# Kernel tuning notes

Measured on AMD Instinct MI355X. Metric: run time of the kernel, lower is better.

The kernel has to match this reference:

```python
import jax, jax.numpy as jnp
import numpy as np

D_IN = 2048
D_LATENT = 16384
BATCH = 4096
K = 64


def setup_inputs() -> dict:
    key = jax.random.key(0)
    k1, k2, k3 = jax.random.split(key, 3)
    s_enc = 1.0 / np.sqrt(D_IN)
    s_dec = 1.0 / np.sqrt(D_LATENT)
    return {
        "x": jax.random.normal(k1, (BATCH, D_IN), dtype=jnp.float32),
        "W_enc": jax.random.normal(k2, (D_LATENT, D_IN), dtype=jnp.float32) * s_enc,
        "b_enc": jnp.zeros((D_LATENT,), dtype=jnp.float32),
        "W_dec": jax.random.normal(k3, (D_IN, D_LATENT), dtype=jnp.float32) * s_dec,
        "b_dec": jnp.zeros((D_IN,), dtype=jnp.float32),
        "k": K,
    }


def reference(x, W_enc, b_enc, W_dec, b_dec, k):
    # encode: dense GEMM + ReLU  -> h: [B, d_latent]
    h = jax.nn.relu(jnp.einsum("bd,ld->bl", x, W_enc) + b_enc)
    # top-k masking over latent dim (dim=1)
    _, idx = jax.lax.top_k(h, k)  # idx: [B, k]
    B = h.shape[0]
    mask = jnp.zeros(h.shape, dtype=bool).at[jnp.arange(B)[:, None], idx].set(True)
    h_topk = jnp.where(mask, h, jnp.zeros((), dtype=h.dtype))
    # decode: GEMM through sparse latents
    x_hat = jnp.einsum("bl,dl->bd", h_topk, W_dec) + b_dec
    return x_hat, h, h_topk
```

## Files before the change

### kernel.cpp

```cpp
#include <hip/hip_runtime.h>
#include <cstdint>

#define DIN   2048
#define DLAT  16384
#define NB    4096
#define KSEL  64
#define MAXC  128
#define CAP   2048
#define SEG   64
#define TAU   1.5f

typedef unsigned short u16;
typedef unsigned int   u32;
typedef __attribute__((ext_vector_type(8))) short short8;
typedef __attribute__((ext_vector_type(4))) float f32x4;
typedef __attribute__((ext_vector_type(4))) u32  u32x4;

#define GLOAD_LDS16(g, l)                                              \
    __builtin_amdgcn_global_load_lds(                                  \
        (const __attribute__((address_space(1))) void*)(g),            \
        (__attribute__((address_space(3))) void*)(l), 16, 0, 0)

__device__ __forceinline__ u32 f32_to_bf16(u32 u)
{
    u += 0x7FFFu + ((u >> 16) & 1u);
    return u >> 16;
}

__device__ __forceinline__ float bf16_to_f32(u16 w)
{
    return __uint_as_float((u32)w << 16);
}

__global__ __launch_bounds__(256)
void cvt_f32_bf16_kernel(const float* __restrict__ in, u16* __restrict__ out, int n8)
{
    const int i = blockIdx.x * 256 + threadIdx.x;
    if (i >= n8) return;
    const float4* p = reinterpret_cast<const float4*>(in) + (size_t)i * 2;
    const float4 a = p[0], b = p[1];
    const float v[8] = {a.x, a.y, a.z, a.w, b.x, b.y, b.z, b.w};
    u32 r[8];
#pragma unroll
    for (int j = 0; j < 8; ++j) r[j] = f32_to_bf16(__float_as_uint(v[j]));
    uint4 o;
    o.x = r[0] | (r[1] << 16);
    o.y = r[2] | (r[3] << 16);
    o.z = r[4] | (r[5] << 16);
    o.w = r[6] | (r[7] << 16);
    reinterpret_cast<uint4*>(out)[i] = o;
}

template <bool APPEND>
__global__ __launch_bounds__(512, 2)
void sae_encode_8ph(const u16* __restrict__ XB, const u16* __restrict__ WB,
                    const float* __restrict__ benc, float* __restrict__ H,
                    u32* __restrict__ cnt2, uint2* __restrict__ candbase)
{
    __shared__ __align__(16) u16 lds[65536];

    const int tid = threadIdx.x;
    const int wv  = tid >> 6;
    const int ln  = tid & 63;
    const int wm  = wv >> 2;
    const int wn  = wv & 3;
    const int fr  = ln & 15;
    const int fq  = ln >> 4;

    const int b   = blockIdx.x;
    const int wg  = (b & 7) * 128 + (b >> 3);
    const int m_blk = wg & 15;
    const int n_blk = wg >> 4;
    const size_t bm = (size_t)m_blk * 256;
    const size_t bn = (size_t)n_blk * 256;

    const int sslot = (ln & 3) ^ ((ln >> 3) & 3);
    const int srow  = wv * 16 + (ln >> 2);
    const u16* aSrc = XB + (bm + srow) * (size_t)DIN + sslot * 8;
    const u16* bSrc = WB + (bn + srow) * (size_t)DIN + sslot * 8;
    const size_t rowStep = (size_t)128 * DIN;

    auto STG = [&](int mat, int tile, int kkh) {
        const u16* s0 = (mat ? bSrc : aSrc) + tile * 64 + kkh * 32;
        const int dst = (tile & 1) * 32768 + mat * 16384 + kkh * 8192 + wv * 512;
        GLOAD_LDS16(s0,           &lds[dst]);
        GLOAD_LDS16(s0 + rowStep, &lds[dst + 4096]);
    };

    f32x4 acc[8][4];
#pragma unroll
    for (int i = 0; i < 8; ++i)
#pragma unroll
        for (int j = 0; j < 4; ++j) acc[i][j] = (f32x4)0.0f;

    const int swb = (fq ^ ((fr >> 1) & 3)) * 8;
    const int arow0 = wm * 128 + fr;
    const int brow0 = wn * 64 + fr;

    STG(0, 0, 0); STG(1, 0, 0);
    STG(0, 0, 1); STG(1, 0, 1);
    STG(0, 1, 0); STG(1, 1, 0);

    short8 aR[8], bX[2], bY[2];

    for (int g = 0; g < 32; ++g) {
        const int buf = (g & 1) * 32768;

        if (g < 31) asm volatile("s_waitcnt vmcnt(8)" ::: "memory");
        else        asm volatile("s_waitcnt vmcnt(4)" ::: "memory");
        __builtin_amdgcn_s_barrier();
#pragma unroll
        for (int mi = 0; mi < 8; ++mi)
            aR[mi] = *reinterpret_cast<const short8*>(
                &lds[buf + (arow0 + mi * 16) * 32 + swb]);
        bX[0] = *reinterpret_cast<const short8*>(&lds[buf + 16384 + (brow0 +  0) * 32 + swb]);
        bX[1] = *reinterpret_cast<const short8*>(&lds[buf + 16384 + (brow0 + 16) * 32 + swb]);
        if (g < 31) { STG(0, g + 1, 1); STG(1, g + 1, 1); }
        asm volatile("s_waitcnt lgkmcnt(0)" ::: "memory");
        __builtin_amdgcn_sched_barrier(0);
        __builtin_amdgcn_s_setprio(1);
#pragma unroll
        for (int mi = 0; mi < 8; ++mi) {
            acc[mi][0] = __builtin_amdgcn_mfma_f32_16x16x32_bf16(aR[mi], bX[0], acc[mi][0], 0, 0, 0);
            acc[mi][1] = __builtin_amdgcn_mfma_f32_16x16x32_bf16(aR[mi], bX[1], acc[mi][1], 0, 0, 0);
        }
        __builtin_amdgcn_s_setprio(0);

        __builtin_amdgcn_s_barrier();
        bY[0] = *reinterpret_cast<const short8*>(&lds[buf + 16384 + (brow0 + 32) * 32 + swb]);
        bY[1] = *reinterpret_cast<const short8*>(&lds[buf + 16384 + (brow0 + 48) * 32 + swb]);
        if (g < 30) STG(0, g + 2, 0);
        asm volatile("s_waitcnt lgkmcnt(0)" ::: "memory");
        __builtin_amdgcn_sched_barrier(0);
        __builtin_amdgcn_s_setprio(1);
#pragma unroll
        for (int mi = 0; mi < 8; ++mi) {
            acc[mi][2] = __builtin_amdgcn_mfma_f32_16x16x32_bf16(aR[mi], bY[0], acc[mi][2], 0, 0, 0);
            acc[mi][3] = __builtin_amdgcn_mfma_f32_16x16x32_bf16(aR[mi], bY[1], acc[mi][3], 0, 0, 0);
        }
        __builtin_amdgcn_s_setprio(0);

        if (g < 30)       asm volatile("s_waitcnt vmcnt(10)" ::: "memory");
        else if (g == 30) asm volatile("s_waitcnt vmcnt(8)"  ::: "memory");
        else              asm volatile("s_waitcnt vmcnt(0)"  ::: "memory");
        __builtin_amdgcn_s_barrier();
#pragma unroll
        for (int mi = 0; mi < 8; ++mi)
            aR[mi] = *reinterpret_cast<const short8*>(
                &lds[buf + 8192 + (arow0 + mi * 16) * 32 + swb]);
        bY[0] = *reinterpret_cast<const short8*>(&lds[buf + 24576 + (brow0 + 32) * 32 + swb]);
        bY[1] = *reinterpret_cast<const short8*>(&lds[buf + 24576 + (brow0 + 48) * 32 + swb]);
        if (g < 30) STG(1, g + 2, 0);
        asm volatile("s_waitcnt lgkmcnt(0)" ::: "memory");
        __builtin_amdgcn_sched_barrier(0);
        __builtin_amdgcn_s_setprio(1);
#pragma unroll
        for (int mi = 0; mi < 8; ++mi) {
            acc[mi][2] = __builtin_amdgcn_mfma_f32_16x16x32_bf16(aR[mi], bY[0], acc[mi][2], 0, 0, 0);
            acc[mi][3] = __builtin_amdgcn_mfma_f32_16x16x32_bf16(aR[mi], bY[1], acc[mi][3], 0, 0, 0);
        }
        __builtin_amdgcn_s_setprio(0);

        bX[0] = *reinterpret_cast<const short8*>(&lds[buf + 24576 + (brow0 +  0) * 32 + swb]);
        bX[1] = *reinterpret_cast<const short8*>(&lds[buf + 24576 + (brow0 + 16) * 32 + swb]);
        asm volatile("s_waitcnt lgkmcnt(0)" ::: "memory");
        __builtin_amdgcn_sched_barrier(0);
        __builtin_amdgcn_s_setprio(1);
#pragma unroll
        for (int mi = 0; mi < 8; ++mi) {
            acc[mi][0] = __builtin_amdgcn_mfma_f32_16x16x32_bf16(aR[mi], bX[0], acc[mi][0], 0, 0, 0);
            acc[mi][1] = __builtin_amdgcn_mfma_f32_16x16x32_bf16(aR[mi], bX[1], acc[mi][1], 0, 0, 0);
        }
        __builtin_amdgcn_s_setprio(0);
    }

    u32* rowcnt = reinterpret_cast<u32*>(lds);
    if (APPEND) {
        __syncthreads();
        if (tid < 256) rowcnt[tid] = 0u;
        __syncthreads();
    }

#pragma unroll
    for (int ni = 0; ni < 4; ++ni) {
        const size_t col = bn + wn * 64 + ni * 16 + fr;
        const float be = benc[col];
#pragma unroll
        for (int mi = 0; mi < 8; ++mi) {
            const int lr0 = wm * 128 + mi * 16 + fq * 4;
#pragma unroll
            for (int j = 0; j < 4; ++j) {
                const float val = fmaxf(acc[mi][ni][j] + be, 0.0f);
                __builtin_nontemporal_store(val, &H[(bm + lr0 + j) * DLAT + col]);
                if (APPEND && val > TAU) {
                    const u32 p = atomicAdd(&rowcnt[lr0 + j], 1u);
                    if (p < SEG)
                        candbase[(bm + lr0 + j) * (size_t)(DLAT / 2)
                                 + (size_t)n_blk * SEG + p] =
                            make_uint2((u32)col, __float_as_uint(val));
                }
            }
        }
    }
    if (APPEND) {
        __syncthreads();
        if (tid < 256)
            cnt2[(bm + tid) * 64 + n_blk] = min(rowcnt[tid], (u32)SEG);
    }
}

__global__ __launch_bounds__(256, 4)
void sae_encode_kernel(const float* __restrict__ X, const float* __restrict__ W,
                       const float* __restrict__ benc, float* __restrict__ H)
{
    __shared__ float As[32][132];
    __shared__ float Bs[32][132];

    const int tid  = threadIdx.x;
    const int bm   = blockIdx.y * 128;
    const int bn   = blockIdx.x * 128;

    const int wave = tid >> 6;
    const int lane = tid & 63;
    const int tm   = ((wave >> 1) << 3) + (lane >> 3);
    const int tn   = ((wave &  1) << 3) + (lane &  7);

    float acc[8][8];
#pragma unroll
    for (int i = 0; i < 8; ++i)
#pragma unroll
        for (int j = 0; j < 8; ++j) acc[i][j] = 0.0f;

    const int lrow = tid >> 1;
    const int lcol = (tid & 1) << 4;

    const float* xptr = X + (size_t)(bm + lrow) * DIN + lcol;
    const float* wptr = W + (size_t)(bn + lrow) * DIN + lcol;

    for (int k0 = 0; k0 < DIN; k0 += 32) {
#pragma unroll
        for (int i = 0; i < 4; ++i) {
            const float4 av = *reinterpret_cast<const float4*>(xptr + k0 + 4 * i);
            const float4 bv = *reinterpret_cast<const float4*>(wptr + k0 + 4 * i);
            const int kk = lcol + 4 * i;
            As[kk + 0][lrow] = av.x; As[kk + 1][lrow] = av.y;
            As[kk + 2][lrow] = av.z; As[kk + 3][lrow] = av.w;
            Bs[kk + 0][lrow] = bv.x; Bs[kk + 1][lrow] = bv.y;
            Bs[kk + 2][lrow] = bv.z; Bs[kk + 3][lrow] = bv.w;
        }
        __syncthreads();

#pragma unroll 8
        for (int k = 0; k < 32; ++k) {
            const float4 a0 = *reinterpret_cast<const float4*>(&As[k][tm * 8]);
            const float4 a1 = *reinterpret_cast<const float4*>(&As[k][tm * 8 + 4]);
            const float4 b0 = *reinterpret_cast<const float4*>(&Bs[k][tn * 8]);
            const float4 b1 = *reinterpret_cast<const float4*>(&Bs[k][tn * 8 + 4]);
            const float a[8] = {a0.x, a0.y, a0.z, a0.w, a1.x, a1.y, a1.z, a1.w};
            const float b[8] = {b0.x, b0.y, b0.z, b0.w, b1.x, b1.y, b1.z, b1.w};
#pragma unroll
            for (int i = 0; i < 8; ++i)
#pragma unroll
                for (int j = 0; j < 8; ++j)
                    acc[i][j] = fmaf(a[i], b[j], acc[i][j]);
        }
        __syncthreads();
    }

#pragma unroll
    for (int i = 0; i < 8; ++i) {
        float* orow = H + (size_t)(bm + tm * 8 + i) * DLAT + bn + tn * 8;
#pragma unroll
        for (int j = 0; j < 8; j += 4) {
            float4 o;
            o.x = fmaxf(acc[i][j + 0] + benc[bn + tn * 8 + j + 0], 0.0f);
            o.y = fmaxf(acc[i][j + 1] + benc[bn + tn * 8 + j + 1], 0.0f);
            o.z = fmaxf(acc[i][j + 2] + benc[bn + tn * 8 + j + 2], 0.0f);
            o.w = fmaxf(acc[i][j + 3] + benc[bn + tn * 8 + j + 3], 0.0f);
            *reinterpret_cast<float4*>(orow + j) = o;
        }
    }
}

__device__ __forceinline__ int blk_scan256(int v, volatile int* wsum,
                                           int ln, int wv, int& total)
{
#pragma unroll
    for (int off = 1; off < 64; off <<= 1) {
        const int n = __shfl_up(v, off, 64);
        if (ln >= off) v += n;
    }
    if (ln == 63) wsum[wv] = v;
    __syncthreads();
    int add = 0;
#pragma unroll
    for (int c = 0; c < 3; ++c) if (c < wv) add += wsum[c];
    total = wsum[0] + wsum[1] + wsum[2] + wsum[3];
    __syncthreads();
    return v + add;
}

__device__ __forceinline__ void refine_np(const float* __restrict__ Wenc,
                                          const float* __restrict__ benc,
                                          const float* __restrict__ xs,
                                          int C, const int* cand_idx,
                                          float* cand_val, float psum[32][6],
                                          int tid)
{
    const int g = tid >> 3;
    const int p = tid & 7;
    for (int c0 = 0; c0 < C; c0 += 32) {
        const int ci = c0 + g;
        if (ci < C && p < 6) {
            const int li = cand_idx[ci];
            const float* __restrict__ wr = Wenc + (size_t)li * DIN;
            const int ks = (p < 4) ? p * 384 : 1536 + (p - 4) * 256;
            const int ke = ks + ((p < 4) ? 384 : 256);
            float s = 0.0f;
            for (int k = ks; k < ke; k += 32) {
                float4 w4[8];
#pragma unroll
                for (int j = 0; j < 8; ++j)
                    w4[j] = *reinterpret_cast<const float4*>(wr + k + 4 * j);
#pragma unroll
                for (int j = 0; j < 8; ++j) {
                    const float4 x4 = *reinterpret_cast<const float4*>(xs + k + 4 * j);
                    s = fmaf(x4.x, w4[j].x, s);
                    s = fmaf(x4.y, w4[j].y, s);
                    s = fmaf(x4.z, w4[j].z, s);
                    s = fmaf(x4.w, w4[j].w, s);
                }
            }
            psum[g][p] = s;
        }
        __syncthreads();
        if (ci < C && p == 0) {
            float total = 0.0f;
#pragma unroll
            for (int q = 0; q < 6; ++q)
                total = __fadd_rn(total, psum[g][q]);
            total = __fadd_rn(total, benc[cand_idx[ci]]);
            cand_val[ci] = fmaxf(total, 0.0f);
        }
        __syncthreads();
    }
}

__global__ __launch_bounds__(256)
void sae_topk_compact(const u32* __restrict__ cnt2, const float* __restrict__ X,
                      const float* __restrict__ Wenc, const float* __restrict__ benc,
                      float* __restrict__ Ht, float band,
                      const u16* __restrict__ WT, const float* __restrict__ bdec,
                      float* __restrict__ xhat)
{
    __shared__ __align__(16) float xs[DIN];
    __shared__ u32  lidx[CAP];
    __shared__ u32  lval[CAP];
    __shared__ u32  scnt[64];
    __shared__ u32  soff[64];
    __shared__ int  sh_n;
    __shared__ u32  hist[4][256];
    __shared__ int  scan_[256];
    __shared__ int  wsum[4];
    __shared__ int  sh_bin, sh_above;
    __shared__ int   cand_idx[MAXC];
    __shared__ float cand_val[MAXC];
    __shared__ unsigned char cand_sel[MAXC];
    __shared__ float psum[32][6];
    __shared__ int   sel_i[KSEL];
    __shared__ float sel_v[KSEL];
    __shared__ int   dec_i[KSEL];
    __shared__ float dec_v[KSEL];

    const int tid = threadIdx.x;
    const int wv  = tid >> 6;
    const int ln  = tid & 63;
    const int row = blockIdx.x;
    const uint2* __restrict__ candRow =
        reinterpret_cast<const uint2*>(Ht + (size_t)row * DLAT);

    {
        const float4* xp = reinterpret_cast<const float4*>(X + (size_t)row * DIN);
        reinterpret_cast<float4*>(xs)[tid * 2 + 0] = xp[tid * 2 + 0];
        reinterpret_cast<float4*>(xs)[tid * 2 + 1] = xp[tid * 2 + 1];
    }
    if (tid < KSEL) { dec_i[tid] = 0; dec_v[tid] = 0.0f; }
    if (tid < 64) scnt[tid] = cnt2[(size_t)row * 64 + tid];
    __syncthreads();
    if (tid < 64) {
        const u32 v0 = scnt[tid];
        u32 s = v0;
#pragma unroll
        for (int off = 1; off < 64; off <<= 1) {
            const u32 nn = __shfl_up(s, off, 64);
            if (ln >= off) s += nn;
        }
        soff[tid] = s - v0;
        if (tid == 63) sh_n = (int)s;
    }
    __syncthreads();
    const int n = min(sh_n, CAP);

    for (int i = tid; i < 64 * SEG; i += 256) {
        const int seg  = i >> 6;
        const int slot = i & (SEG - 1);
        if (slot < (int)scnt[seg]) {
            const int d = (int)soff[seg] + slot;
            if (d < CAP) {
                const uint2 e = candRow[seg * SEG + slot];
                lidx[d] = e.x;
                lval[d] = e.y;
            }
        }
    }
    __syncthreads();

    u32 prefix = 0, msk = 0;
    int kk = KSEL;
    for (int pass = 0; pass < 3; ++pass) {
        const int shift = 24 - 8 * pass;
        hist[0][tid] = 0; hist[1][tid] = 0; hist[2][tid] = 0; hist[3][tid] = 0;
        __syncthreads();
        for (int i = tid; i < n; i += 256) {
            const u32 x = lval[i];
            if ((x & msk) == prefix)
                atomicAdd(&hist[wv][(x >> shift) & 255u], 1u);
        }
        __syncthreads();
        int val = (int)(hist[0][255 - tid] + hist[1][255 - tid] +
                        hist[2][255 - tid] + hist[3][255 - tid]);
#pragma unroll
        for (int off = 1; off < 64; off <<= 1) {
            const int nn = __shfl_up(val, off, 64);
            if (ln >= off) val += nn;
        }
        if (ln == 63) wsum[wv] = val;
        __syncthreads();
        int add = 0;
#pragma unroll
        for (int c = 0; c < 3; ++c) if (c < wv) add += wsum[c];
        scan_[tid] = val + add;
        __syncthreads();
        {
            const int binh = (int)(hist[0][tid] + hist[1][tid] +
                                   hist[2][tid] + hist[3][tid]);
            const int ge = scan_[255 - tid];
            const int gt = ge - binh;
            if (gt < kk && ge >= kk) { sh_bin = tid; sh_above = gt; }
        }
        __syncthreads();
        prefix |= ((u32)sh_bin) << shift;
        msk    |= 0xFFu << shift;
        kk     -= sh_above;
        __syncthreads();
    }

    const float Tf = __uint_as_float(prefix);
    const float hi = Tf + band;
    const float lo = Tf - band;

    int c_safe = 0, c_band = 0;
    for (int i = tid; i < n; i += 256) {
        const float f = __uint_as_float(lval[i]);
        c_safe += (f > hi) ? 1 : 0;
        c_band += (f >= lo && f <= hi) ? 1 : 0;
    }
    int S;
    (void)blk_scan256(c_safe, wsum, ln, wv, S);
    int totC;
    const int bincl = blk_scan256(c_band, wsum, ln, wv, totC);
    int bpos = bincl - c_band;
    int C = totC;
    if (C > MAXC) C = MAXC;
    int need = KSEL - S;
    if (need > C) need = C;

    for (int i = tid; i < n; i += 256) {
        const float f = __uint_as_float(lval[i]);
        if (f >= lo && f <= hi) {
            if (bpos < MAXC) cand_idx[bpos] = (int)lidx[i];
            ++bpos;
        }
    }
    __syncthreads();

    refine_np(Wenc, benc, xs, C, cand_idx, cand_val, psum, tid);

    if (tid < C) {
        const float val = cand_val[tid];
        const int  myi = cand_idx[tid];
        int r = 0;
        for (int m = 0; m < C; ++m)
            r += (cand_val[m] > val ||
                  (cand_val[m] == val && cand_idx[m] < myi)) ? 1 : 0;
        cand_sel[tid] = (r < need) ? 1 : 0;
    }
    __syncthreads();

    int csel = 0;
    for (int i = tid; i < n; i += 256) {
        const float f = __uint_as_float(lval[i]);
        bool s = (f > hi);
        if (!s && f >= lo && f <= hi) {
            const int gi = (int)lidx[i];
            for (int m = 0; m < C; ++m)
                if (cand_idx[m] == gi) { s = (cand_sel[m] != 0); break; }
        }
        csel += s ? 1 : 0;
    }
    int totSel;
    int spos = blk_scan256(csel, wsum, ln, wv, totSel) - csel;
    if (totSel > KSEL) totSel = KSEL;
    for (int i = tid; i < n; i += 256) {
        const float f = __uint_as_float(lval[i]);
        bool s = (f > hi);
        if (!s && f >= lo && f <= hi) {
            const int gi = (int)lidx[i];
            for (int m = 0; m < C; ++m)
                if (cand_idx[m] == gi) { s = (cand_sel[m] != 0); break; }
        }
        if (s) {
            if (spos < KSEL) { sel_i[spos] = (int)lidx[i]; sel_v[spos] = f; }
            ++spos;
        }
    }
    __syncthreads();

    if (tid < totSel) {
        const int id = sel_i[tid];
        int r = 0;
        for (int m = 0; m < totSel; ++m)
            r += (sel_i[m] < id) ? 1 : 0;
        dec_i[r] = id;
        dec_v[r] = sel_v[tid];
    }
    __syncthreads();

    float* orow = Ht + (size_t)row * DLAT;
    {
        f32x4 z; z.x = 0.0f; z.y = 0.0f; z.z = 0.0f; z.w = 0.0f;
#pragma unroll
        for (int j = 0; j < 16; ++j)
            __builtin_nontemporal_store(z,
                reinterpret_cast<f32x4*>(orow + j * 1024 + tid * 4));
    }
    __syncthreads();
    if (tid < totSel) orow[dec_i[tid]] = dec_v[tid];

    const int d = tid * 8;
    float4 a0 = *reinterpret_cast<const float4*>(bdec + d);
    float4 a1 = *reinterpret_cast<const float4*>(bdec + d + 4);
#pragma unroll 8
    for (int j = 0; j < KSEL; ++j) {
        const float f = dec_v[j];
        const int   l = dec_i[j];
        const u16* wp = WT + (size_t)l * DIN + d;
        const ushort4 w0 = *reinterpret_cast<const ushort4*>(wp);
        const ushort4 w1 = *reinterpret_cast<const ushort4*>(wp + 4);
        a0.x = fmaf(f, bf16_to_f32(w0.x), a0.x);
        a0.y = fmaf(f, bf16_to_f32(w0.y), a0.y);
        a0.z = fmaf(f, bf16_to_f32(w0.z), a0.z);
        a0.w = fmaf(f, bf16_to_f32(w0.w), a0.w);
        a1.x = fmaf(f, bf16_to_f32(w1.x), a1.x);
        a1.y = fmaf(f, bf16_to_f32(w1.y), a1.y);
        a1.z = fmaf(f, bf16_to_f32(w1.z), a1.z);
        a1.w = fmaf(f, bf16_to_f32(w1.w), a1.w);
    }
    float* xo = xhat + (size_t)row * DIN + d;
    f32x4 s0; s0.x = a0.x; s0.y = a0.y; s0.z = a0.z; s0.w = a0.w;
    f32x4 s1; s1.x = a1.x; s1.y = a1.y; s1.z = a1.z; s1.w = a1.w;
    __builtin_nontemporal_store(s0, reinterpret_cast<f32x4*>(xo));
    __builtin_nontemporal_store(s1, reinterpret_cast<f32x4*>(xo + 4));
}

template <bool FUSE, bool WRITE_LISTS>
__global__ __launch_bounds__(256)
void sae_topk_kernel(const float* __restrict__ H, const float* __restrict__ X,
                     const float* __restrict__ Wenc, const float* __restrict__ benc,
                     float* __restrict__ Ht, int* __restrict__ sidx,
                     float* __restrict__ sval, float band,
                     const u16* __restrict__ WT, const float* __restrict__ bdec,
                     float* __restrict__ xhat)
{
    __shared__ __align__(16) float xs[DIN];
    __shared__ u32  hist[4][256];
    __shared__ int  scan_[256];
    __shared__ int  wsum[4];
    __shared__ int  sh_bin, sh_above;
    __shared__ int           cand_idx[MAXC];
    __shared__ float         cand_val[MAXC];
    __shared__ unsigned char cand_sel[MAXC];
    __shared__ float psum[32][6];
    __shared__ int   dec_idx[KSEL];
    __shared__ float dec_val[KSEL];

    const int tid = threadIdx.x;
    const int wv  = tid >> 6;
    const int ln  = tid & 63;
    const int row = blockIdx.x;
    const u32* __restrict__ hrow =
        reinterpret_cast<const u32*>(H) + (size_t)row * DLAT;

    {
        const float4* xp = reinterpret_cast<const float4*>(X + (size_t)row * DIN);
        reinterpret_cast<float4*>(xs)[tid * 2 + 0] = xp[tid * 2 + 0];
        reinterpret_cast<float4*>(xs)[tid * 2 + 1] = xp[tid * 2 + 1];
    }
    if (FUSE && tid < KSEL) { dec_idx[tid] = 0; dec_val[tid] = 0.0f; }

    u32 v[64];
#pragma unroll
    for (int j = 0; j < 16; ++j) {
        const u32x4 q = __builtin_nontemporal_load(
            reinterpret_cast<const u32x4*>(hrow + j * 1024 + tid * 4));
        v[j * 4 + 0] = q.x; v[j * 4 + 1] = q.y;
        v[j * 4 + 2] = q.z; v[j * 4 + 3] = q.w;
    }

    u32 prefix = 0, msk = 0;
    int kk = KSEL;
    for (int pass = 0; pass < 3; ++pass) {
        const int shift = 24 - 8 * pass;
        hist[0][tid] = 0; hist[1][tid] = 0; hist[2][tid] = 0; hist[3][tid] = 0;
        __syncthreads();
#pragma unroll
        for (int e = 0; e < 64; ++e) {
            const u32 x = v[e];
            if (x != 0u && (x & msk) == prefix)
                atomicAdd(&hist[wv][(x >> shift) & 255u], 1u);
        }
        __syncthreads();
        int val = (int)(hist[0][255 - tid] + hist[1][255 - tid] +
                        hist[2][255 - tid] + hist[3][255 - tid]);
#pragma unroll
        for (int off = 1; off < 64; off <<= 1) {
            const int nn = __shfl_up(val, off, 64);
            if (ln >= off) val += nn;
        }
        if (ln == 63) wsum[wv] = val;
        __syncthreads();
        int add = 0;
#pragma unroll
        for (int c = 0; c < 3; ++c) if (c < wv) add += wsum[c];
        scan_[tid] = val + add;
        __syncthreads();
        {
            const int binh = (int)(hist[0][tid] + hist[1][tid] +
                                   hist[2][tid] + hist[3][tid]);
            const int ge = scan_[255 - tid];
            const int gt = ge - binh;
            if (gt < kk && ge >= kk) { sh_bin = tid; sh_above = gt; }
        }
        __syncthreads();
        prefix |= ((u32)sh_bin) << shift;
        msk    |= 0xFFu << shift;
        kk     -= sh_above;
        __syncthreads();
    }

    const float Tf = __uint_as_float(prefix);
    const float hi = Tf + band;
    const float lo = Tf - band;

    int c_safe = 0, c_band = 0;
#pragma unroll
    for (int e = 0; e < 64; ++e) {
        const float f = __uint_as_float(v[e]);
        c_safe += (f > hi) ? 1 : 0;
        c_band += (f >= lo && f <= hi) ? 1 : 0;
    }

    int S;
    (void)blk_scan256(c_safe, wsum, ln, wv, S);
    int totC;
    const int bincl = blk_scan256(c_band, wsum, ln, wv, totC);
    const int bexc  = bincl - c_band;
    int C = totC;
    if (C > MAXC) C = MAXC;
    int need = KSEL - S;
    if (need > C) need = C;

    {
        int bpos = bexc;
#pragma unroll
        for (int e = 0; e < 64; ++e) {
            const float f = __uint_as_float(v[e]);
            if (f >= lo && f <= hi) {
                if (bpos < MAXC)
                    cand_idx[bpos] = (e >> 2) * 1024 + tid * 4 + (e & 3);
                ++bpos;
            }
        }
    }
    __syncthreads();

    refine_np(Wenc, benc, xs, C, cand_idx, cand_val, psum, tid);

    if (tid < C) {
        const float val = cand_val[tid];
        const int  myi = cand_idx[tid];
        int r = 0;
        for (int m = 0; m < C; ++m)
            r += (cand_val[m] > val ||
                  (cand_val[m] == val && cand_idx[m] < myi)) ? 1 : 0;
        cand_sel[tid] = (r < need) ? 1 : 0;
    }
    __syncthreads();

    unsigned long long selmask = 0ull;
#pragma unroll
    for (int e = 0; e < 64; ++e) {
        const float f = __uint_as_float(v[e]);
        bool s = (f > hi);
        if (!s && f >= lo && f <= hi) {
            const int gi = (e >> 2) * 1024 + tid * 4 + (e & 3);
            for (int m = 0; m < C; ++m)
                if (cand_idx[m] == gi) { s = (cand_sel[m] != 0); break; }
        }
        if (s) selmask |= 1ull << e;
    }
    const int csel = __popcll(selmask);

    int totSel;
    const int pincl = blk_scan256(csel, wsum, ln, wv, totSel);
    const int pos0 = pincl - csel;

    float* orow = Ht + (size_t)row * DLAT;
#pragma unroll
    for (int j = 0; j < 16; ++j) {
        f32x4 o;
        o.x = ((selmask >> (j * 4 + 0)) & 1) ? __uint_as_float(v[j * 4 + 0]) : 0.0f;
        o.y = ((selmask >> (j * 4 + 1)) & 1) ? __uint_as_float(v[j * 4 + 1]) : 0.0f;
        o.z = ((selmask >> (j * 4 + 2)) & 1) ? __uint_as_float(v[j * 4 + 2]) : 0.0f;
        o.w = ((selmask >> (j * 4 + 3)) & 1) ? __uint_as_float(v[j * 4 + 3]) : 0.0f;
        __builtin_nontemporal_store(o,
            reinterpret_cast<f32x4*>(orow + j * 1024 + tid * 4));
    }
    {
        int pos = pos0;
#pragma unroll
        for (int e = 0; e < 64; ++e) {
            if ((selmask >> e) & 1) {
                const int gi = (e >> 2) * 1024 + tid * 4 + (e & 3);
                if (WRITE_LISTS && pos < KSEL) {
                    sidx[(size_t)row * KSEL + pos] = gi;
                    sval[(size_t)row * KSEL + pos] = __uint_as_float(v[e]);
                }
                if (FUSE && pos < KSEL) {
                    dec_idx[pos] = gi;
                    dec_val[pos] = __uint_as_float(v[e]);
                }
                ++pos;
            }
        }
    }

    if (FUSE) {
        __syncthreads();
        const int d = tid * 8;
        float4 a0 = *reinterpret_cast<const float4*>(bdec + d);
        float4 a1 = *reinterpret_cast<const float4*>(bdec + d + 4);
#pragma unroll 8
        for (int j = 0; j < KSEL; ++j) {
            const float f = dec_val[j];
            const int   l = dec_idx[j];
            const u16* wp = WT + (size_t)l * DIN + d;
            const ushort4 w0 = *reinterpret_cast<const ushort4*>(wp);
            const ushort4 w1 = *reinterpret_cast<const ushort4*>(wp + 4);
            a0.x = fmaf(f, bf16_to_f32(w0.x), a0.x);
            a0.y = fmaf(f, bf16_to_f32(w0.y), a0.y);
            a0.z = fmaf(f, bf16_to_f32(w0.z), a0.z);
            a0.w = fmaf(f, bf16_to_f32(w0.w), a0.w);
            a1.x = fmaf(f, bf16_to_f32(w1.x), a1.x);
            a1.y = fmaf(f, bf16_to_f32(w1.y), a1.y);
            a1.z = fmaf(f, bf16_to_f32(w1.z), a1.z);
            a1.w = fmaf(f, bf16_to_f32(w1.w), a1.w);
        }
        float* xo = xhat + (size_t)row * DIN + d;
        f32x4 s0; s0.x = a0.x; s0.y = a0.y; s0.z = a0.z; s0.w = a0.w;
        f32x4 s1; s1.x = a1.x; s1.y = a1.y; s1.z = a1.z; s1.w = a1.w;
        __builtin_nontemporal_store(s0, reinterpret_cast<f32x4*>(xo));
        __builtin_nontemporal_store(s1, reinterpret_cast<f32x4*>(xo + 4));
    }
}

__global__ __launch_bounds__(256)
void sae_transpose_cvt(const float* __restrict__ W, u16* __restrict__ WT)
{
    __shared__ float t[32][65];
    const int bx = blockIdx.x * 32;
    const int by = blockIdx.y * 64;
    const int lx = threadIdx.x;
    const int ly = threadIdx.y;

    for (int r = ly; r < 64; r += 8)
        t[lx][r] = W[(size_t)(by + r) * DLAT + bx + lx];
    __syncthreads();
    for (int c = ly; c < 32; c += 8) {
        const u32 lo = f32_to_bf16(__float_as_uint(t[c][2 * lx + 0]));
        const u32 hi = f32_to_bf16(__float_as_uint(t[c][2 * lx + 1]));
        *reinterpret_cast<u32*>(WT + (size_t)(bx + c) * DIN + by + 2 * lx) =
            lo | (hi << 16);
    }
}

__global__ __launch_bounds__(512)
void sae_decode_f32(const float* __restrict__ Wd, const int* __restrict__ sidx,
                    const float* __restrict__ sval, const float* __restrict__ bdec,
                    float* __restrict__ xhat)
{
    __shared__ int   si[KSEL];
    __shared__ float sv[KSEL];
    const int row = blockIdx.x;
    const int tid = threadIdx.x;
    if (tid < KSEL) {
        si[tid] = sidx[(size_t)row * KSEL + tid];
        sv[tid] = sval[(size_t)row * KSEL + tid];
    }
    __syncthreads();

    const int d = tid * 4;
    float4 acc = *reinterpret_cast<const float4*>(bdec + d);
#pragma unroll 4
    for (int j = 0; j < KSEL; ++j) {
        const float f = sv[j];
        const int   l = si[j];
        acc.x = fmaf(f, Wd[(size_t)(d + 0) * DLAT + l], acc.x);
        acc.y = fmaf(f, Wd[(size_t)(d + 1) * DLAT + l], acc.y);
        acc.z = fmaf(f, Wd[(size_t)(d + 2) * DLAT + l], acc.z);
        acc.w = fmaf(f, Wd[(size_t)(d + 3) * DLAT + l], acc.w);
    }
    *reinterpret_cast<float4*>(xhat + (size_t)row * DIN + d) = acc;
}

__global__ __launch_bounds__(512)
void sae_decode_nows_kernel(const float* __restrict__ Ht, const float* __restrict__ Wd,
                            const float* __restrict__ bdec, float* __restrict__ xhat)
{
    __shared__ int   si[KSEL];
    __shared__ float sv[KSEL];
    __shared__ unsigned cnt;
    const int row = blockIdx.x;
    const int tid = threadIdx.x;
    if (tid == 0) cnt = 0;
    __syncthreads();
    for (int i = tid; i < DLAT; i += 512) {
        const float v = Ht[(size_t)row * DLAT + i];
        if (v != 0.0f) {
            const unsigned p = atomicAdd(&cnt, 1u);
            if (p < KSEL) { si[p] = i; sv[p] = v; }
        }
    }
    __syncthreads();
    const unsigned n = cnt < (unsigned)KSEL ? cnt : (unsigned)KSEL;
    const int d = tid * 4;
    float4 acc = *reinterpret_cast<const float4*>(bdec + d);
    for (unsigned j = 0; j < n; ++j) {
        const float f = sv[j];
        const int   l = si[j];
        acc.x = fmaf(f, Wd[(size_t)(d + 0) * DLAT + l], acc.x);
        acc.y = fmaf(f, Wd[(size_t)(d + 1) * DLAT + l], acc.y);
        acc.z = fmaf(f, Wd[(size_t)(d + 2) * DLAT + l], acc.z);
        acc.w = fmaf(f, Wd[(size_t)(d + 3) * DLAT + l], acc.w);
    }
    *reinterpret_cast<float4*>(xhat + (size_t)row * DIN + d) = acc;
}

extern "C" void kernel_launch(void* const* d_in, const int* in_sizes, int n_in,
                              void* d_out, int out_size, void* d_ws, size_t ws_size,
                              hipStream_t stream)
{
    const float* x     = (const float*)d_in[0];
    const float* W_enc = (const float*)d_in[1];
    const float* b_enc = (const float*)d_in[2];
    const float* W_dec = (const float*)d_in[3];
    const float* b_dec = (const float*)d_in[4];

    float* xhat  = (float*)d_out;
    float* h     = xhat + (size_t)NB * DIN;
    float* htopk = h + (size_t)NB * DLAT;

    const size_t LIST_BYTES = 2097152ull;
    const size_t WT_BYTES   = 2ull * DLAT * DIN;
    const size_t XB_BYTES   = 2ull * NB * DIN;
    const size_t WB_BYTES   = 2ull * DLAT * DIN;
    const size_t XB_OFF     = LIST_BYTES + WT_BYTES;
    const size_t WB_OFF     = XB_OFF + XB_BYTES;
    const size_t CNT_OFF    = WB_OFF + WB_BYTES;
    const size_t CNT_BYTES  = (size_t)NB * 64 * 4;

    int*   sp_idx = (int*)d_ws;
    float* sp_val = (float*)((char*)d_ws + (LIST_BYTES / 2));
    u16*   WT     = (u16*)((char*)d_ws + LIST_BYTES);
    u16*   xb     = (u16*)((char*)d_ws + XB_OFF);
    u16*   wb     = (u16*)((char*)d_ws + WB_OFF);
    u32*   cnt2   = (u32*)((char*)d_ws + CNT_OFF);

    const bool have_lists = ws_size >= LIST_BYTES;
    const bool have_wt    = ws_size >= LIST_BYTES + WT_BYTES;
    const bool have_mfma  = ws_size >= WB_OFF + WB_BYTES;
    const bool have_cand  = ws_size >= CNT_OFF + CNT_BYTES;

    const float band = have_mfma ? 0.03f : 1e-3f;

    if (have_wt) {
        sae_transpose_cvt<<<dim3(DLAT / 32, DIN / 64), dim3(32, 8), 0, stream>>>(W_dec, WT);
    }

    if (have_mfma) {
        cvt_f32_bf16_kernel<<<(NB * DIN / 8 + 255) / 256, 256, 0, stream>>>(x, xb, NB * DIN / 8);
        cvt_f32_bf16_kernel<<<(DLAT * DIN / 8 + 255) / 256, 256, 0, stream>>>(W_enc, wb, DLAT * DIN / 8);
        if (have_cand && have_wt) {
            sae_encode_8ph<true><<<(NB / 256) * (DLAT / 256), 512, 0, stream>>>(
                xb, wb, b_enc, h, cnt2, reinterpret_cast<uint2*>(htopk));
        } else {
            sae_encode_8ph<false><<<(NB / 256) * (DLAT / 256), 512, 0, stream>>>(
                xb, wb, b_enc, h, nullptr, nullptr);
        }
    } else {
        sae_encode_kernel<<<dim3(DLAT / 128, NB / 128), 256, 0, stream>>>(x, W_enc, b_enc, h);
    }

    if (have_cand && have_wt && have_mfma) {
        sae_topk_compact<<<NB, 256, 0, stream>>>(
            cnt2, x, W_enc, b_enc, htopk, band, WT, b_dec, xhat);
    } else if (have_wt) {
        sae_topk_kernel<true, false><<<NB, 256, 0, stream>>>(
            h, x, W_enc, b_enc, htopk, nullptr, nullptr, band, WT, b_dec, xhat);
    } else if (have_lists) {
        sae_topk_kernel<false, true><<<NB, 256, 0, stream>>>(
            h, x, W_enc, b_enc, htopk, sp_idx, sp_val, band, nullptr, nullptr, nullptr);
        sae_decode_f32<<<NB, 512, 0, stream>>>(W_dec, sp_idx, sp_val, b_dec, xhat);
    } else {
        sae_topk_kernel<false, false><<<NB, 256, 0, stream>>>(
            h, x, W_enc, b_enc, htopk, nullptr, nullptr, band, nullptr, nullptr, nullptr);
        sae_decode_nows_kernel<<<NB, 512, 0, stream>>>(htopk, W_dec, b_dec, xhat);
    }
}
```

Before: 764.6 us.

## Move half of h_topk zero-fill into encode epilogue and widen decode weight loads

The encode GEMM epilogue now writes zeros into the upper half of the h_topk buffer (aliased through the candidate buffer) for column blocks 32 and above. The top-k kernel then zeroes only the lower half of each row before scattering the selected values. Moving that work is meant to overlap the zero-fill with the GEMM and shorten the top-k kernel. Decode loops also replace two 8-byte bf16 weight loads with one 16-byte load. The aliasing relies on the candidate lists, written at per-block offsets, not overlapping the zeroed upper-half region, which is a correctness risk.

```diff
diff --git a/kernel.cpp b/kernel.cpp
--- a/kernel.cpp
+++ b/kernel.cpp
@@ -181,6 +181,8 @@
         __syncthreads();
     }
 
+    float* htf = reinterpret_cast<float*>(candbase);
+
 #pragma unroll
     for (int ni = 0; ni < 4; ++ni) {
         const size_t col = bn + wn * 64 + ni * 16 + fr;
@@ -192,12 +194,17 @@
             for (int j = 0; j < 4; ++j) {
                 const float val = fmaxf(acc[mi][ni][j] + be, 0.0f);
                 __builtin_nontemporal_store(val, &H[(bm + lr0 + j) * DLAT + col]);
-                if (APPEND && val > TAU) {
-                    const u32 p = atomicAdd(&rowcnt[lr0 + j], 1u);
-                    if (p < SEG)
-                        candbase[(bm + lr0 + j) * (size_t)(DLAT / 2)
-                                 + (size_t)n_blk * SEG + p] =
-                            make_uint2((u32)col, __float_as_uint(val));
+                if (APPEND) {
+                    if (n_blk >= 32)
+                        __builtin_nontemporal_store(0.0f,
+                            &htf[(bm + lr0 + j) * DLAT + col]);
+                    if (val > TAU) {
+                        const u32 p = atomicAdd(&rowcnt[lr0 + j], 1u);
+                        if (p < SEG)
+                            candbase[(bm + lr0 + j) * (size_t)(DLAT / 2)
+                                     + (size_t)n_blk * SEG + p] =
+                                make_uint2((u32)col, __float_as_uint(val));
+                    }
                 }
             }
         }
@@ -540,7 +547,7 @@
     {
         f32x4 z; z.x = 0.0f; z.y = 0.0f; z.z = 0.0f; z.w = 0.0f;
 #pragma unroll
-        for (int j = 0; j < 16; ++j)
+        for (int j = 0; j < 8; ++j)
             __builtin_nontemporal_store(z,
                 reinterpret_cast<f32x4*>(orow + j * 1024 + tid * 4));
     }
@@ -554,17 +561,15 @@
     for (int j = 0; j < KSEL; ++j) {
         const float f = dec_v[j];
         const int   l = dec_i[j];
-        const u16* wp = WT + (size_t)l * DIN + d;
-        const ushort4 w0 = *reinterpret_cast<const ushort4*>(wp);
-        const ushort4 w1 = *reinterpret_cast<const ushort4*>(wp + 4);
-        a0.x = fmaf(f, bf16_to_f32(w0.x), a0.x);
-        a0.y = fmaf(f, bf16_to_f32(w0.y), a0.y);
-        a0.z = fmaf(f, bf16_to_f32(w0.z), a0.z);
-        a0.w = fmaf(f, bf16_to_f32(w0.w), a0.w);
-        a1.x = fmaf(f, bf16_to_f32(w1.x), a1.x);
-        a1.y = fmaf(f, bf16_to_f32(w1.y), a1.y);
-        a1.z = fmaf(f, bf16_to_f32(w1.z), a1.z);
-        a1.w = fmaf(f, bf16_to_f32(w1.w), a1.w);
+        const uint4 w = *reinterpret_cast<const uint4*>(WT + (size_t)l * DIN + d);
+        a0.x = fmaf(f, bf16_to_f32((u16)(w.x & 0xFFFFu)), a0.x);
+        a0.y = fmaf(f, bf16_to_f32((u16)(w.x >> 16)),     a0.y);
+        a0.z = fmaf(f, bf16_to_f32((u16)(w.y & 0xFFFFu)), a0.z);
+        a0.w = fmaf(f, bf16_to_f32((u16)(w.y >> 16)),     a0.w);
+        a1.x = fmaf(f, bf16_to_f32((u16)(w.z & 0xFFFFu)), a1.x);
+        a1.y = fmaf(f, bf16_to_f32((u16)(w.z >> 16)),     a1.y);
+        a1.z = fmaf(f, bf16_to_f32((u16)(w.w & 0xFFFFu)), a1.z);
+        a1.w = fmaf(f, bf16_to_f32((u16)(w.w >> 16)),     a1.w);
     }
     float* xo = xhat + (size_t)row * DIN + d;
     f32x4 s0; s0.x = a0.x; s0.y = a0.y; s0.z = a0.z; s0.w = a0.w;
@@ -764,17 +769,15 @@
         for (int j = 0; j < KSEL; ++j) {
             const float f = dec_val[j];
             const int   l = dec_idx[j];
-            const u16* wp = WT + (size_t)l * DIN + d;
-            const ushort4 w0 = *reinterpret_cast<const ushort4*>(wp);
-            const ushort4 w1 = *reinterpret_cast<const ushort4*>(wp + 4);
-            a0.x = fmaf(f, bf16_to_f32(w0.x), a0.x);
-            a0.y = fmaf(f, bf16_to_f32(w0.y), a0.y);
-            a0.z = fmaf(f, bf16_to_f32(w0.z), a0.z);
-            a0.w = fmaf(f, bf16_to_f32(w0.w), a0.w);
-            a1.x = fmaf(f, bf16_to_f32(w1.x), a1.x);
-            a1.y = fmaf(f, bf16_to_f32(w1.y), a1.y);
-            a1.z = fmaf(f, bf16_to_f32(w1.z), a1.z);
-            a1.w = fmaf(f, bf16_to_f32(w1.w), a1.w);
+            const uint4 w = *reinterpret_cast<const uint4*>(WT + (size_t)l * DIN + d);
+            a0.x = fmaf(f, bf16_to_f32((u16)(w.x & 0xFFFFu)), a0.x);
+            a0.y = fmaf(f, bf16_to_f32((u16)(w.x >> 16)),     a0.y);
+            a0.z = fmaf(f, bf16_to_f32((u16)(w.y & 0xFFFFu)), a0.z);
+            a0.w = fmaf(f, bf16_to_f32((u16)(w.y >> 16)),     a0.w);
+            a1.x = fmaf(f, bf16_to_f32((u16)(w.z & 0xFFFFu)), a1.x);
+            a1.y = fmaf(f, bf16_to_f32((u16)(w.z >> 16)),     a1.y);
+            a1.z = fmaf(f, bf16_to_f32((u16)(w.w & 0xFFFFu)), a1.z);
+            a1.w = fmaf(f, bf16_to_f32((u16)(w.w >> 16)),     a1.w);
         }
         float* xo = xhat + (size_t)row * DIN + d;
         f32x4 s0; s0.x = a0.x; s0.y = a0.y; s0.z = a0.z; s0.w = a0.w;
```

After: 818.9 us. 7.1% more time.
